# Performance work log

Measured on AMD Instinct MI355X. Metric: run time of the kernel, lower is better.

The kernel has to match this reference:

```python
import jax, jax.numpy as jnp
import numpy as np

D_MODEL = 128
D_STATE = 16
KCONV = 3
SQUEEZE = 16
NEIGH = 27
D_INNER = 2 * D_MODEL            # 256
C_CONV = D_INNER // SQUEEZE      # 16 conv3d output channels
D_SEQ = C_CONV * NEIGH           # 432 selective-scan channel dim
DT_RANK = int(np.ceil((D_MODEL // SQUEEZE * NEIGH) / 16))  # 14
LN_EPS = 1e-5


def setup_inputs() -> dict:
    key = jax.random.key(0)
    ks = jax.random.split(key, 10)
    B, Dd, H, W = 2, 16, 16, 16
    x = jax.random.normal(ks[0], (B, Dd, H, W, D_MODEL), dtype=jnp.float32)
    w_in = jax.random.normal(ks[1], (2 * D_INNER, D_MODEL), dtype=jnp.float32) * 0.02
    conv_w = jax.random.normal(ks[2], (C_CONV, SQUEEZE, KCONV, KCONV, KCONV), dtype=jnp.float32) * 0.05
    conv_b = jnp.zeros((C_CONV,), dtype=jnp.float32)
    x_proj_w = jax.random.normal(ks[3], (DT_RANK + 2 * D_STATE, D_SEQ), dtype=jnp.float32) * 0.05
    s = DT_RANK ** -0.5
    dt_w = jax.random.uniform(ks[4], (D_SEQ, DT_RANK), minval=-s, maxval=s, dtype=jnp.float32)
    # dt bias = inverse-softplus of dt ~ LogUniform[1e-3, 0.1]
    dt = jnp.exp(jax.random.uniform(ks[5], (D_SEQ,), dtype=jnp.float32)
                 * (np.log(0.1) - np.log(1e-3)) + np.log(1e-3))
    dt_b = dt + jnp.log(-jnp.expm1(-dt))
    A_logs = jnp.broadcast_to(jnp.log(jnp.arange(1, D_STATE + 1, dtype=jnp.float32)),
                              (D_SEQ, D_STATE)).copy()
    Ds = jnp.ones((D_SEQ,), dtype=jnp.float32)
    w_fold = jax.random.normal(ks[6], (D_INNER, D_SEQ), dtype=jnp.float32) * 0.05
    ln_g = jnp.ones((D_INNER,), dtype=jnp.float32)
    ln_b = jnp.zeros((D_INNER,), dtype=jnp.float32)
    w_out = jax.random.normal(ks[7], (D_MODEL, D_INNER), dtype=jnp.float32) * 0.05
    return dict(x=x, w_in=w_in, conv_w=conv_w, conv_b=conv_b, x_proj_w=x_proj_w,
                dt_w=dt_w, dt_b=dt_b, A_logs=A_logs, Ds=Ds, w_fold=w_fold,
                ln_g=ln_g, ln_b=ln_b, w_out=w_out)


def _selective_scan(u, delta, A, Bm, Cm, Dskip, delta_bias):
    # u, delta: (B, Dch, L); A: (Dch, N); Bm, Cm: (B, N, L); Dskip: (Dch,)
    delta = jax.nn.softplus(delta + delta_bias[None, :, None])
    a = jnp.exp(delta[..., None] * A[None, :, None, :])                     # (B,Dch,L,N)
    b = (delta * u)[..., None] * jnp.swapaxes(Bm, 1, 2)[:, None, :, :]      # (B,Dch,L,N)

    def combine(c1, c2):
        a1, b1 = c1
        a2, b2 = c2
        return a1 * a2, a2 * b1 + b2

    _, h = jax.lax.associative_scan(combine, (a, b), axis=2)                # (B,Dch,L,N)
    y = jnp.einsum('bdln,bnl->bdl', h, Cm)
    return y + Dskip[None, :, None] * u


def _unfold3(x):
    # x: (B, C, D, H, W) -> (B, C*27, D, H, W), channel-major, offset-minor
    B, C, Dd, H, W = x.shape
    p = KCONV // 2
    xp = jnp.pad(x, ((0, 0), (0, 0), (p, p), (p, p), (p, p)))
    taps = jnp.stack([xp[:, :, i:i + Dd, j:j + H, k:k + W]
                      for i in range(KCONV) for j in range(KCONV) for k in range(KCONV)],
                     axis=2)  # (B, C, 27, D, H, W)
    return taps.reshape(B, C * NEIGH, Dd, H, W)


def _forward(x, w_in, conv_w, conv_b, x_proj_w, dt_w, dt_b, A_logs, Ds,
             w_fold, ln_g, ln_b, w_out):
    B, Dd, H, W, _ = x.shape
    L = Dd * H * W
    xz = x @ w_in.T                                   # (B,D,H,W,512)
    xp, z = jnp.split(xz, 2, axis=-1)
    xc = jnp.transpose(xp, (0, 4, 1, 2, 3))           # (B,256,D,H,W)
    xc = jax.lax.conv_general_dilated(
        xc, conv_w, window_strides=(1, 1, 1), padding='SAME',
        dimension_numbers=('NCDHW', 'OIDHW', 'NCDHW'),
        feature_group_count=C_CONV) + conv_b[None, :, None, None, None]
    xc = jax.nn.silu(xc)                              # (B,16,D,H,W)
    xu = _unfold3(xc)                                 # (B,432,D,H,W)
    xs = xu.reshape(B, D_SEQ, L)
    x_dbl = jnp.einsum('bdl,cd->bcl', xs, x_proj_w)   # (B,46,L)
    dts = x_dbl[:, :DT_RANK]
    Bm = x_dbl[:, DT_RANK:DT_RANK + D_STATE]
    Cm = x_dbl[:, DT_RANK + D_STATE:]
    dts = jnp.einsum('brl,dr->bdl', dts, dt_w)        # (B,432,L)
    A = -jnp.exp(A_logs)
    y = _selective_scan(xs, dts, A, Bm, Cm, Ds, dt_b)  # (B,432,L)
    y = jnp.swapaxes(y, 1, 2).reshape(B, Dd, H, W, D_SEQ)
    y = y @ w_fold.T                                   # (B,D,H,W,256)
    mu = jnp.mean(y, axis=-1, keepdims=True)
    var = jnp.var(y, axis=-1, keepdims=True)
    y = (y - mu) * jax.lax.rsqrt(var + LN_EPS) * ln_g + ln_b
    y = y * jax.nn.silu(z)
    return y @ w_out.T                                 # (B,D,H,W,128)


def reference(x, w_in, conv_w, conv_b, x_proj_w, dt_w, dt_b, A_logs, Ds,
              w_fold, ln_g, ln_b, w_out):
    return _forward(x, w_in, conv_w, conv_b, x_proj_w, dt_w, dt_b, A_logs, Ds,
                    w_fold, ln_g, ln_b, w_out)
```

## Files before the change

### kernel.cpp

```cpp
#include <hip/hip_runtime.h>
#include <hip/hip_bf16.h>

#define DM     128
#define DSTATE 16
#define DINNER 256
#define CCONV  16
#define NEIGH  27
#define DSEQ   432
#define DTRANK 14
#define LVOL   4096
#define BATCH  2
#define NTOK   8192

typedef __attribute__((ext_vector_type(8))) unsigned short ushort8_t;
typedef __attribute__((ext_vector_type(8))) short short8_t;
typedef __attribute__((ext_vector_type(4))) float f32x4_t;

__device__ __forceinline__ float bf2f(unsigned short u) {
    union { unsigned int i; float f; } v; v.i = ((unsigned int)u) << 16; return v.f;
}
__device__ __forceinline__ unsigned short f2b(float f) {
    __hip_bfloat16 hb = __float2bfloat16(f);
    return *(unsigned short*)&hb;
}

__global__ void k_wprep(const float* __restrict__ w_in, const float* __restrict__ w_fold,
                        const float* __restrict__ w_out, const float* __restrict__ x_proj_w,
                        float2* __restrict__ wint2, unsigned short* __restrict__ wfb,
                        unsigned short* __restrict__ wob, unsigned short* __restrict__ wxpb) {
    int idx = blockIdx.x * 256 + threadIdx.x;
    if (idx < 32768) {
        int j = idx >> 8, t = idx & 255;
        wint2[idx] = make_float2(w_in[t * 128 + j], w_in[(t + 256) * 128 + j]);
    } else if (idx < 32768 + 114688) {
        int local = idx - 32768;
        int o = local / 448, dk = local - o * 448;
        wfb[local] = (dk < 432) ? f2b(w_fold[o * 432 + dk]) : (unsigned short)0;
    } else if (idx < 32768 + 114688 + 32768) {
        int local = idx - 32768 - 114688;
        wob[local] = f2b(w_out[local]);
    } else if (idx < 32768 + 114688 + 32768 + 21504) {
        int local = idx - 32768 - 114688 - 32768;
        int c = local / 448, dk = local - c * 448;
        wxpb[local] = (c < 46 && dk < 432) ? f2b(x_proj_w[c * 432 + dk]) : (unsigned short)0;
    }
}

__global__ void k_inproj(const float* __restrict__ x, const float2* __restrict__ wint2,
                         float* __restrict__ xpt, float* __restrict__ zbuf) {
    int t = threadIdx.x;
    int tokbase = blockIdx.x * 16;
    int b = tokbase >> 12, lb = tokbase & 4095;
    __shared__ float xs_[16][128];
    for (int idx = t; idx < 2048; idx += 256)
        xs_[idx >> 7][idx & 127] = x[tokbase * 128 + idx];
    __syncthreads();
    float a0[16], a1[16];
#pragma unroll
    for (int k = 0; k < 16; k++) { a0[k] = 0.f; a1[k] = 0.f; }
    for (int j = 0; j < 128; j += 4) {
        float2 w0 = wint2[(j + 0) * 256 + t];
        float2 w1 = wint2[(j + 1) * 256 + t];
        float2 w2 = wint2[(j + 2) * 256 + t];
        float2 w3 = wint2[(j + 3) * 256 + t];
#pragma unroll
        for (int k = 0; k < 16; k++) {
            float4 xv = *(const float4*)&xs_[k][j];
            a0[k] += xv.x * w0.x + xv.y * w1.x + xv.z * w2.x + xv.w * w3.x;
            a1[k] += xv.x * w0.y + xv.y * w1.y + xv.z * w2.y + xv.w * w3.y;
        }
    }
    float* xr = xpt + (size_t)(b * 256 + t) * 4096 + lb;
#pragma unroll
    for (int k = 0; k < 16; k++) xr[k] = a0[k];
#pragma unroll
    for (int k = 0; k < 16; k++) zbuf[(tokbase + k) * 256 + t] = a1[k];
}

__global__ void k_conv(const float* __restrict__ xpt, const float* __restrict__ conv_w,
                       const float* __restrict__ conv_b, float* __restrict__ xc) {
    int t = threadIdx.x;
    int tok = blockIdx.x * 256 + t;
    int co = blockIdx.y;
    int b = tok >> 12, l = tok & 4095;
    int d0 = l >> 8, h0 = (l >> 4) & 15, w0 = l & 15;
    int nbo[27];
#pragma unroll
    for (int t27 = 0; t27 < 27; t27++) {
        int di = t27 / 9 - 1, dj = (t27 / 3) % 3 - 1, dk = t27 % 3 - 1;
        int zd = d0 + di, zh = h0 + dj, zw = w0 + dk;
        nbo[t27] = ((unsigned)zd > 15u || (unsigned)zh > 15u || (unsigned)zw > 15u)
                   ? -1 : ((zd << 8) + (zh << 4) + zw);
    }
    const float* xb = xpt + (size_t)(b * 256 + co * 16) * 4096;
    const float* wr = conv_w + co * 432;
    float acc0 = conv_b[co], acc1 = 0.f;
    for (int t27 = 0; t27 < 27; t27++) {
        int o = nbo[t27];
        if (o >= 0) {
#pragma unroll
            for (int q = 0; q < 16; q += 2) {
                acc0 += xb[q * 4096 + o]       * wr[q * 27 + t27];
                acc1 += xb[(q + 1) * 4096 + o] * wr[(q + 1) * 27 + t27];
            }
        }
    }
    float acc = acc0 + acc1;
    acc = acc / (1.f + __expf(-acc));
    xc[(b * 16 + co) * 4096 + l] = acc;
}

__global__ void k_xdbl(const float* __restrict__ xc, const unsigned short* __restrict__ wxpb,
                       float* __restrict__ dts, __hip_bfloat16* __restrict__ bc2) {
    int t = threadIdx.x;
    int w = t >> 6, l = t & 63;
    int lc = l & 15, lr = l >> 4;
    int tokbase = blockIdx.x * 32;
    int b = tokbase >> 12, lbase = tokbase & 4095;

    __shared__ unsigned short xsT[32][456];

    for (int p = t; p < 432; p += 256) {
        int ch = p / 27, tap = p - ch * 27;
        int di = tap / 9 - 1, dj = (tap / 3) % 3 - 1, dk = tap % 3 - 1;
        const float* xr = xc + (size_t)(b * 16 + ch) * 4096;
        for (int tk = 0; tk < 32; tk++) {
            int ll = lbase + tk;
            int zd = (ll >> 8) + di, zh = ((ll >> 4) & 15) + dj, zw = (ll & 15) + dk;
            float v = (((unsigned)zd <= 15u) && ((unsigned)zh <= 15u) && ((unsigned)zw <= 15u))
                      ? xr[(zd << 8) + (zh << 4) + zw] : 0.f;
            xsT[tk][p] = f2b(v);
        }
    }
    for (int idx = t; idx < 16 * 32; idx += 256)
        xsT[idx & 31][432 + (idx >> 5)] = 0;
    __syncthreads();

    for (int ti = w; ti < 6; ti += 4) {
        int mt = ti % 3, nt = ti / 3;
        f32x4_t acc = (f32x4_t){0.f, 0.f, 0.f, 0.f};
        for (int ks = 0; ks < 14; ks++) {
            int kb = ks * 32 + lr * 8;
            short8_t bfr = *(const short8_t*)&xsT[nt * 16 + lc][kb];
            short8_t afr = *(const short8_t*)(wxpb + (size_t)(mt * 16 + lc) * 448 + kb);
            acc = __builtin_amdgcn_mfma_f32_16x16x32_bf16(afr, bfr, acc, 0, 0, 0);
        }
        int ltok = lbase + nt * 16 + lc;
#pragma unroll
        for (int r = 0; r < 4; r++) {
            int c = mt * 16 + lr * 4 + r;
            if (c < 14)
                dts[(size_t)(b * 14 + c) * 4096 + ltok] = acc[r];
            else if (c < 46)
                bc2[(size_t)(b * 32 + (c - 14)) * 4096 + ltok] = __float2bfloat16(acc[r]);
        }
    }
}

__global__ __launch_bounds__(512, 2) void k_scan(
        const float* __restrict__ xc, const float* __restrict__ dts,
        const unsigned short* __restrict__ bc2, const float* __restrict__ dt_w,
        const float* __restrict__ dt_b, const float* __restrict__ A_logs,
        const float* __restrict__ Ds, unsigned short* __restrict__ y) {
    int bd = blockIdx.x;
    int b = bd / 432, dch = bd % 432;
    int t = threadIdx.x;
    int lane = t & 63, wv = t >> 6;

    bool intA = true;
#pragma unroll
    for (int n = 0; n < 16; n++) {
        float An = -__expf(A_logs[dch * 16 + n]);
        intA = intA && (fabsf(An + (float)(n + 1)) < 1e-3f);
    }
    float Dskip = Ds[dch];

    int cch = dch / 27, t27 = dch % 27;
    int di = t27 / 9 - 1, dj = (t27 / 3) % 3 - 1, dk = t27 % 3 - 1;

    float dtv[8];
    {
        float s[8];
        float bias = dt_b[dch];
#pragma unroll
        for (int i = 0; i < 8; i++) s[i] = bias;
        const float* dsb = dts + (size_t)(b * 14) * 4096 + t * 8;
#pragma unroll
        for (int r = 0; r < 14; r++) {
            float d8[8];
            *(float4*)&d8[0] = *(const float4*)(dsb + (size_t)r * 4096);
            *(float4*)&d8[4] = *(const float4*)(dsb + (size_t)r * 4096 + 4);
            float w = dt_w[dch * 14 + r];
#pragma unroll
            for (int i = 0; i < 8; i++) s[i] += d8[i] * w;
        }
#pragma unroll
        for (int i = 0; i < 8; i++)
            dtv[i] = (s[i] > 15.f) ? s[i] : log1pf(__expf(s[i]));
    }

    int d0 = t >> 5, h0 = (t >> 1) & 15, w0 = (t & 1) << 3;
    int zd = d0 + di, zh = h0 + dj;
    bool rowok = ((unsigned)zd <= 15u) && ((unsigned)zh <= 15u);
    const float* xr = xc + (size_t)(b * 16 + cch) * 4096 + (zd << 8) + (zh << 4);
    float dtu[8], ys[8];
#pragma unroll
    for (int i = 0; i < 8; i++) {
        int zw = w0 + i + dk;
        float u = (rowok && (unsigned)zw <= 15u) ? xr[zw] : 0.f;
        dtu[i] = dtv[i] * u;
        ys[i] = Dskip * u;
    }

    const unsigned short* bcb = bc2 + (size_t)(b * 32) * 4096 + t * 8;

    __shared__ float waggA[8][16], waggB[8][16];
    __shared__ float waggS[8];

    float h[16];
    float av[8];

    if (intA) {
        float aw[8];
#pragma unroll
        for (int i = 0; i < 8; i++) { av[i] = __expf(-dtv[i]); aw[i] = av[i]; }
        float sdt = ((dtv[0] + dtv[1]) + (dtv[2] + dtv[3]))
                  + ((dtv[4] + dtv[5]) + (dtv[6] + dtv[7]));

        float Bp[16];
        {
            ushort8_t Bnx = *(const ushort8_t*)(bcb);
#pragma unroll
            for (int n = 0; n < 16; n++) {
                ushort8_t Bv = Bnx;
                if (n < 15) Bnx = *(const ushort8_t*)(bcb + (size_t)(n + 1) * 4096);
                float bp = 0.f;
#pragma unroll
                for (int i = 0; i < 8; i++)
                    bp = aw[i] * bp + dtu[i] * bf2f(Bv[i]);
                Bp[n] = bp;
                if (n < 15) {
#pragma unroll
                    for (int i = 0; i < 8; i++) aw[i] *= av[i];
                }
            }
        }

#pragma unroll
        for (int s = 1; s < 64; s <<= 1) {
            float psdt = __shfl_up(sdt, s, 64);
            float pl = __expf(-sdt);
            float pb[16];
#pragma unroll
            for (int n = 0; n < 16; n++) pb[n] = __shfl_up(Bp[n], s, 64);
            if (lane >= s) {
                float pw = pl;
#pragma unroll
                for (int n = 0; n < 16; n++) {
                    Bp[n] = pw * pb[n] + Bp[n];
                    pw *= pl;
                }
                sdt += psdt;
            }
        }

        if (lane == 63) {
            waggS[wv] = sdt;
#pragma unroll
            for (int n = 0; n < 16; n++) waggB[wv][n] = Bp[n];
        }
        __syncthreads();

        float exsdt = __shfl_up(sdt, 1, 64);
        float exB[16];
#pragma unroll
        for (int n = 0; n < 16; n++) exB[n] = __shfl_up(Bp[n], 1, 64);
        if (lane == 0) {
            exsdt = 0.f;
#pragma unroll
            for (int n = 0; n < 16; n++) exB[n] = 0.f;
        }
        float WB[16];
#pragma unroll
        for (int n = 0; n < 16; n++) WB[n] = 0.f;
        for (int ww = 0; ww < wv; ww++) {
            float plw = __expf(-waggS[ww]);
            float pww = plw;
#pragma unroll
            for (int n = 0; n < 16; n++) {
                WB[n] = pww * WB[n] + waggB[ww][n];
                pww *= plw;
            }
        }
        float pex = __expf(-exsdt);
        float pwx = pex;
#pragma unroll
        for (int n = 0; n < 16; n++) {
            h[n] = pwx * WB[n] + exB[n];
            pwx *= pex;
        }
    } else {
        float A[16];
#pragma unroll
        for (int n = 0; n < 16; n++) A[n] = -__expf(A_logs[dch * 16 + n]);
        float Ap[16], Bp[16];
        ushort8_t Bnx = *(const ushort8_t*)(bcb);
#pragma unroll
        for (int n = 0; n < 16; n++) {
            ushort8_t Bv = Bnx;
            if (n < 15) Bnx = *(const ushort8_t*)(bcb + (size_t)(n + 1) * 4096);
            float ap = 1.f, bp = 0.f, An = A[n];
#pragma unroll
            for (int i = 0; i < 8; i++) {
                float a = __expf(dtv[i] * An);
                bp = a * bp + dtu[i] * bf2f(Bv[i]);
                ap *= a;
            }
            Ap[n] = ap; Bp[n] = bp;
        }
#pragma unroll
        for (int s = 1; s < 64; s <<= 1) {
#pragma unroll
            for (int n = 0; n < 16; n++) {
                float pa = __shfl_up(Ap[n], s, 64);
                float pb = __shfl_up(Bp[n], s, 64);
                if (lane >= s) {
                    Bp[n] = Ap[n] * pb + Bp[n];
                    Ap[n] *= pa;
                }
            }
        }
        if (lane == 63) {
#pragma unroll
            for (int n = 0; n < 16; n++) { waggA[wv][n] = Ap[n]; waggB[wv][n] = Bp[n]; }
        }
        __syncthreads();
#pragma unroll
        for (int n = 0; n < 16; n++) {
            float exA = __shfl_up(Ap[n], 1, 64);
            float exB = __shfl_up(Bp[n], 1, 64);
            if (lane == 0) { exA = 1.f; exB = 0.f; }
            float WB = 0.f;
            for (int ww = 0; ww < wv; ww++)
                WB = waggA[ww][n] * WB + waggB[ww][n];
            h[n] = exA * WB + exB;
        }
    }

    if (intA) {
        float aw[8];
#pragma unroll
        for (int i = 0; i < 8; i++) aw[i] = av[i];
        ushort8_t Bnx = *(const ushort8_t*)(bcb);
        ushort8_t Cnx = *(const ushort8_t*)(bcb + (size_t)16 * 4096);
#pragma unroll
        for (int n = 0; n < 16; n++) {
            ushort8_t Bv = Bnx, Cv = Cnx;
            if (n < 15) {
                Bnx = *(const ushort8_t*)(bcb + (size_t)(n + 1) * 4096);
                Cnx = *(const ushort8_t*)(bcb + (size_t)(17 + n) * 4096);
            }
            float hn = h[n];
#pragma unroll
            for (int i = 0; i < 8; i++) {
                hn = aw[i] * hn + dtu[i] * bf2f(Bv[i]);
                ys[i] += hn * bf2f(Cv[i]);
            }
            if (n < 15) {
#pragma unroll
                for (int i = 0; i < 8; i++) aw[i] *= av[i];
            }
        }
    } else {
        ushort8_t Bnx = *(const ushort8_t*)(bcb);
        ushort8_t Cnx = *(const ushort8_t*)(bcb + (size_t)16 * 4096);
#pragma unroll
        for (int n = 0; n < 16; n++) {
            float An = -__expf(A_logs[dch * 16 + n]);
            ushort8_t Bv = Bnx, Cv = Cnx;
            if (n < 15) {
                Bnx = *(const ushort8_t*)(bcb + (size_t)(n + 1) * 4096);
                Cnx = *(const ushort8_t*)(bcb + (size_t)(17 + n) * 4096);
            }
            float hn = h[n];
#pragma unroll
            for (int i = 0; i < 8; i++) {
                float a = __expf(dtv[i] * An);
                hn = a * hn + dtu[i] * bf2f(Bv[i]);
                ys[i] += hn * bf2f(Cv[i]);
            }
        }
    }

    unsigned short* yo = y + (size_t)(b * 432 + dch) * 4096 + t * 8;
    ushort8_t o8;
#pragma unroll
    for (int i = 0; i < 8; i++) o8[i] = f2b(ys[i]);
    *(ushort8_t*)yo = o8;
}

__global__ void k_tail(const unsigned short* __restrict__ y, const float* __restrict__ zbuf,
                       const unsigned short* __restrict__ wfb, const float* __restrict__ ln_g,
                       const float* __restrict__ ln_b, const unsigned short* __restrict__ wob,
                       float* __restrict__ out) {
    int t = threadIdx.x;
    int w = t >> 6;
    int l = t & 63;
    int lc = l & 15;
    int lr = l >> 4;
    int tokbase = blockIdx.x * 16;
    int b = tokbase >> 12, lbase = tokbase & 4095;

    __shared__ unsigned short Yt[16][456];
    __shared__ unsigned short Pt[16][264];
    __shared__ float red[4][16][2];

    for (int d = t; d < 448; d += 256) {
        if (d < 432) {
            const unsigned short* yr = y + (size_t)(b * 432 + d) * 4096 + lbase;
            ushort8_t v0 = *(const ushort8_t*)(yr);
            ushort8_t v1 = *(const ushort8_t*)(yr + 8);
#pragma unroll
            for (int j = 0; j < 8; j++) { Yt[j][d] = v0[j]; Yt[8 + j][d] = v1[j]; }
        } else {
#pragma unroll
            for (int j = 0; j < 16; j++) Yt[j][d] = 0;
        }
    }
    __syncthreads();

    f32x4_t acc[4];
#pragma unroll
    for (int m = 0; m < 4; m++) acc[m] = (f32x4_t){0.f, 0.f, 0.f, 0.f};
    for (int ks = 0; ks < 14; ks++) {
        int kb = ks * 32 + lr * 8;
        short8_t bf = *(const short8_t*)&Yt[lc][kb];
#pragma unroll
        for (int m = 0; m < 4; m++) {
            int outrow = (4 * w + m) * 16 + lc;
            short8_t af = *(const short8_t*)(wfb + (size_t)outrow * 448 + kb);
            acc[m] = __builtin_amdgcn_mfma_f32_16x16x32_bf16(af, bf, acc[m], 0, 0, 0);
        }
    }

    {
        float s = 0.f, s2 = 0.f;
#pragma unroll
        for (int m = 0; m < 4; m++) {
#pragma unroll
            for (int r = 0; r < 4; r++) { float v = acc[m][r]; s += v; s2 += v * v; }
        }
        s  += __shfl_xor(s, 16, 64);  s2 += __shfl_xor(s2, 16, 64);
        s  += __shfl_xor(s, 32, 64);  s2 += __shfl_xor(s2, 32, 64);
        if (l < 16) { red[w][l][0] = s; red[w][l][1] = s2; }
    }
    __syncthreads();
    float mu, rs;
    {
        float ts  = red[0][lc][0] + red[1][lc][0] + red[2][lc][0] + red[3][lc][0];
        float ts2 = red[0][lc][1] + red[1][lc][1] + red[2][lc][1] + red[3][lc][1];
        mu = ts * (1.f / 256.f);
        float var = ts2 * (1.f / 256.f) - mu * mu;
        rs = rsqrtf(var + 1e-5f);
    }

#pragma unroll
    for (int m = 0; m < 4; m++) {
#pragma unroll
        for (int r = 0; r < 4; r++) {
            int oidx = (4 * w + m) * 16 + lr * 4 + r;
            float g = ln_g[oidx], be = ln_b[oidx];
            float zv = zbuf[(tokbase + lc) * 256 + oidx];
            float sz = zv / (1.f + __expf(-zv));
            float p = ((acc[m][r] - mu) * rs * g + be) * sz;
            Pt[lc][oidx] = f2b(p);
        }
    }
    __syncthreads();

    f32x4_t oacc[2];
    oacc[0] = (f32x4_t){0.f, 0.f, 0.f, 0.f};
    oacc[1] = (f32x4_t){0.f, 0.f, 0.f, 0.f};
    for (int ks = 0; ks < 8; ks++) {
        int kb = ks * 32 + lr * 8;
        short8_t bf = *(const short8_t*)&Pt[lc][kb];
#pragma unroll
        for (int m = 0; m < 2; m++) {
            int orow = (2 * w + m) * 16 + lc;
            short8_t af = *(const short8_t*)(wob + (size_t)orow * 256 + kb);
            oacc[m] = __builtin_amdgcn_mfma_f32_16x16x32_bf16(af, bf, oacc[m], 0, 0, 0);
        }
    }
#pragma unroll
    for (int m = 0; m < 2; m++) {
        float o4[4];
#pragma unroll
        for (int r = 0; r < 4; r++) o4[r] = oacc[m][r];
        *(float4*)&out[(size_t)(tokbase + lc) * 128 + (2 * w + m) * 16 + lr * 4] = *(float4*)o4;
    }
}

extern "C" void kernel_launch(void* const* d_in, const int* in_sizes, int n_in,
                              void* d_out, int out_size, void* d_ws, size_t ws_size,
                              hipStream_t stream) {
    const float* x        = (const float*)d_in[0];
    const float* w_in     = (const float*)d_in[1];
    const float* conv_w   = (const float*)d_in[2];
    const float* conv_b   = (const float*)d_in[3];
    const float* x_proj_w = (const float*)d_in[4];
    const float* dt_w     = (const float*)d_in[5];
    const float* dt_b     = (const float*)d_in[6];
    const float* A_logs   = (const float*)d_in[7];
    const float* Ds       = (const float*)d_in[8];
    const float* w_fold   = (const float*)d_in[9];
    const float* ln_g     = (const float*)d_in[10];
    const float* ln_b     = (const float*)d_in[11];
    const float* w_out    = (const float*)d_in[12];
    float* out = (float*)d_out;

    float* ws     = (float*)d_ws;
    float* xpt    = ws;
    float* zbuf   = xpt    + 2097152;
    float* xc     = zbuf   + 2097152;
    float* dts    = xc     + 131072;
    float* bc2    = dts    + 114688;
    float* ybuf   = bc2    + 262144;
    float* wint   = ybuf   + 3538944;
    float* wfb    = wint   + 65536;
    float* wob    = wfb    + 57344;
    float* wxpb   = wob    + 16384;

    k_wprep<<<dim3(788), dim3(256), 0, stream>>>(w_in, w_fold, w_out, x_proj_w,
                                                 (float2*)wint, (unsigned short*)wfb,
                                                 (unsigned short*)wob, (unsigned short*)wxpb);
    k_inproj<<<dim3(NTOK / 16), dim3(256), 0, stream>>>(x, (const float2*)wint, xpt, zbuf);
    k_conv<<<dim3(NTOK / 256, CCONV), dim3(256), 0, stream>>>(xpt, conv_w, conv_b, xc);
    k_xdbl<<<dim3(NTOK / 32), dim3(256), 0, stream>>>(xc, (const unsigned short*)wxpb,
                                                      dts, (__hip_bfloat16*)bc2);
    k_scan<<<dim3(BATCH * DSEQ), dim3(512), 0, stream>>>(xc, dts, (const unsigned short*)bc2,
                                                         dt_w, dt_b, A_logs, Ds,
                                                         (unsigned short*)ybuf);
    k_tail<<<dim3(NTOK / 16), dim3(256), 0, stream>>>((const unsigned short*)ybuf, zbuf,
                                                      (const unsigned short*)wfb, ln_g, ln_b,
                                                      (const unsigned short*)wob, out);
}
```

Baseline: 142.3 us.

## Use bf16 MFMA for input projection and store z channel-major

The input projection moves from an FP32 scalar FMA loop to bf16 MFMA 16x16x32 instructions. Weights are pre-converted to bf16 and activations are converted to bf16 in shared memory, with 32 tokens per block. The z output is now written channel-major, and the tail kernel reads it with the matching new indexing. This aims to cut the compute cost of the in-projection, at the cost of bf16 precision and a different memory access pattern for z in the tail.

```diff
diff --git a/kernel.cpp b/kernel.cpp
--- a/kernel.cpp
+++ b/kernel.cpp
@@ -26,55 +26,68 @@
 
 __global__ void k_wprep(const float* __restrict__ w_in, const float* __restrict__ w_fold,
                         const float* __restrict__ w_out, const float* __restrict__ x_proj_w,
-                        float2* __restrict__ wint2, unsigned short* __restrict__ wfb,
+                        unsigned short* __restrict__ wib, unsigned short* __restrict__ wfb,
                         unsigned short* __restrict__ wob, unsigned short* __restrict__ wxpb) {
     int idx = blockIdx.x * 256 + threadIdx.x;
-    if (idx < 32768) {
-        int j = idx >> 8, t = idx & 255;
-        wint2[idx] = make_float2(w_in[t * 128 + j], w_in[(t + 256) * 128 + j]);
-    } else if (idx < 32768 + 114688) {
-        int local = idx - 32768;
+    if (idx < 65536) {
+        wib[idx] = f2b(w_in[idx]);
+    } else if (idx < 65536 + 114688) {
+        int local = idx - 65536;
         int o = local / 448, dk = local - o * 448;
         wfb[local] = (dk < 432) ? f2b(w_fold[o * 432 + dk]) : (unsigned short)0;
-    } else if (idx < 32768 + 114688 + 32768) {
-        int local = idx - 32768 - 114688;
+    } else if (idx < 65536 + 114688 + 32768) {
+        int local = idx - 65536 - 114688;
         wob[local] = f2b(w_out[local]);
-    } else if (idx < 32768 + 114688 + 32768 + 21504) {
-        int local = idx - 32768 - 114688 - 32768;
+    } else if (idx < 65536 + 114688 + 32768 + 21504) {
+        int local = idx - 65536 - 114688 - 32768;
         int c = local / 448, dk = local - c * 448;
         wxpb[local] = (c < 46 && dk < 432) ? f2b(x_proj_w[c * 432 + dk]) : (unsigned short)0;
     }
 }
 
-__global__ void k_inproj(const float* __restrict__ x, const float2* __restrict__ wint2,
-                         float* __restrict__ xpt, float* __restrict__ zbuf) {
+__global__ void k_inproj(const float* __restrict__ x, const unsigned short* __restrict__ wib,
+                         float* __restrict__ xpt, float* __restrict__ zbufT) {
     int t = threadIdx.x;
-    int tokbase = blockIdx.x * 16;
-    int b = tokbase >> 12, lb = tokbase & 4095;
-    __shared__ float xs_[16][128];
-    for (int idx = t; idx < 2048; idx += 256)
-        xs_[idx >> 7][idx & 127] = x[tokbase * 128 + idx];
+    int w = t >> 6, l = t & 63;
+    int lc = l & 15, lr = l >> 4;
+    int tokbase = blockIdx.x * 32;
+    int b = tokbase >> 12, lbase = tokbase & 4095;
+
+    __shared__ unsigned short xsT[32][136];
+
+    for (int idx = t; idx < 1024; idx += 256) {
+        int row = idx >> 5, cb = idx & 31;
+        float4 v = *(const float4*)(x + (size_t)(tokbase + row) * 128 + cb * 4);
+        unsigned int p0 = (unsigned)f2b(v.x) | ((unsigned)f2b(v.y) << 16);
+        unsigned int p1 = (unsigned)f2b(v.z) | ((unsigned)f2b(v.w) << 16);
+        *(unsigned int*)&xsT[row][cb * 4]     = p0;
+        *(unsigned int*)&xsT[row][cb * 4 + 2] = p1;
+    }
     __syncthreads();
-    float a0[16], a1[16];
-#pragma unroll
-    for (int k = 0; k < 16; k++) { a0[k] = 0.f; a1[k] = 0.f; }
-    for (int j = 0; j < 128; j += 4) {
-        float2 w0 = wint2[(j + 0) * 256 + t];
-        float2 w1 = wint2[(j + 1) * 256 + t];
-        float2 w2 = wint2[(j + 2) * 256 + t];
-        float2 w3 = wint2[(j + 3) * 256 + t];
-#pragma unroll
-        for (int k = 0; k < 16; k++) {
-            float4 xv = *(const float4*)&xs_[k][j];
-            a0[k] += xv.x * w0.x + xv.y * w1.x + xv.z * w2.x + xv.w * w3.x;
-            a1[k] += xv.x * w0.y + xv.y * w1.y + xv.z * w2.y + xv.w * w3.y;
-        }
-    }
-    float* xr = xpt + (size_t)(b * 256 + t) * 4096 + lb;
-#pragma unroll
-    for (int k = 0; k < 16; k++) xr[k] = a0[k];
-#pragma unroll
-    for (int k = 0; k < 16; k++) zbuf[(tokbase + k) * 256 + t] = a1[k];
+
+#pragma unroll
+    for (int mi = 0; mi < 8; mi++) {
+        int mt = w * 8 + mi;
+#pragma unroll
+        for (int nt = 0; nt < 2; nt++) {
+            f32x4_t acc = (f32x4_t){0.f, 0.f, 0.f, 0.f};
+#pragma unroll
+            for (int ks = 0; ks < 4; ks++) {
+                int kb = ks * 32 + lr * 8;
+                short8_t bfr = *(const short8_t*)&xsT[nt * 16 + lc][kb];
+                short8_t afr = *(const short8_t*)(wib + (size_t)(mt * 16 + lc) * 128 + kb);
+                acc = __builtin_amdgcn_mfma_f32_16x16x32_bf16(afr, bfr, acc, 0, 0, 0);
+            }
+            int ltok = lbase + nt * 16 + lc;
+            int ch = mt * 16 + lr * 4;
+            float* dst = (mt < 16)
+                ? (xpt   + (size_t)(b * 256 + ch)       * 4096 + ltok)
+                : (zbufT + (size_t)(b * 256 + ch - 256) * 4096 + ltok);
+#pragma unroll
+            for (int r = 0; r < 4; r++)
+                dst[(size_t)r * 4096] = acc[r];
+        }
+    }
 }
 
 __global__ void k_conv(const float* __restrict__ xpt, const float* __restrict__ conv_w,
@@ -399,7 +412,7 @@
     *(ushort8_t*)yo = o8;
 }
 
-__global__ void k_tail(const unsigned short* __restrict__ y, const float* __restrict__ zbuf,
+__global__ void k_tail(const unsigned short* __restrict__ y, const float* __restrict__ zbufT,
                        const unsigned short* __restrict__ wfb, const float* __restrict__ ln_g,
                        const float* __restrict__ ln_b, const unsigned short* __restrict__ wob,
                        float* __restrict__ out) {
@@ -470,7 +483,7 @@
         for (int r = 0; r < 4; r++) {
             int oidx = (4 * w + m) * 16 + lr * 4 + r;
             float g = ln_g[oidx], be = ln_b[oidx];
-            float zv = zbuf[(tokbase + lc) * 256 + oidx];
+            float zv = zbufT[(size_t)(b * 256 + oidx) * 4096 + lbase + lc];
             float sz = zv / (1.f + __expf(-zv));
             float p = ((acc[m][r] - mu) * rs * g + be) * sz;
             Pt[lc][oidx] = f2b(p);
@@ -520,27 +533,28 @@
 
     float* ws     = (float*)d_ws;
     float* xpt    = ws;
-    float* zbuf   = xpt    + 2097152;
-    float* xc     = zbuf   + 2097152;
+    float* zbufT  = xpt    + 2097152;
+    float* xc     = zbufT  + 2097152;
     float* dts    = xc     + 131072;
     float* bc2    = dts    + 114688;
     float* ybuf   = bc2    + 262144;
-    float* wint   = ybuf   + 3538944;
-    float* wfb    = wint   + 65536;
+    float* wib    = ybuf   + 3538944;
+    float* wfb    = wib    + 32768;
     float* wob    = wfb    + 57344;
     float* wxpb   = wob    + 16384;
 
-    k_wprep<<<dim3(788), dim3(256), 0, stream>>>(w_in, w_fold, w_out, x_proj_w,
-                                                 (float2*)wint, (unsigned short*)wfb,
+    k_wprep<<<dim3(916), dim3(256), 0, stream>>>(w_in, w_fold, w_out, x_proj_w,
+                                                 (unsigned short*)wib, (unsigned short*)wfb,
                                                  (unsigned short*)wob, (unsigned short*)wxpb);
-    k_inproj<<<dim3(NTOK / 16), dim3(256), 0, stream>>>(x, (const float2*)wint, xpt, zbuf);
+    k_inproj<<<dim3(NTOK / 32), dim3(256), 0, stream>>>(x, (const unsigned short*)wib,
+                                                        xpt, zbufT);
     k_conv<<<dim3(NTOK / 256, CCONV), dim3(256), 0, stream>>>(xpt, conv_w, conv_b, xc);
     k_xdbl<<<dim3(NTOK / 32), dim3(256), 0, stream>>>(xc, (const unsigned short*)wxpb,
                                                       dts, (__hip_bfloat16*)bc2);
     k_scan<<<dim3(BATCH * DSEQ), dim3(512), 0, stream>>>(xc, dts, (const unsigned short*)bc2,
                                                          dt_w, dt_b, A_logs, Ds,
                                                          (unsigned short*)ybuf);
-    k_tail<<<dim3(NTOK / 16), dim3(256), 0, stream>>>((const unsigned short*)ybuf, zbuf,
+    k_tail<<<dim3(NTOK / 16), dim3(256), 0, stream>>>((const unsigned short*)ybuf, zbufT,
                                                       (const unsigned short*)wfb, ln_g, ln_b,
                                                       (const unsigned short*)wob, out);
 }
```

New measurement: 127.3 us. -10.5%, faster.
